# Optimization experiments

Measured on AMD Instinct MI355X. Metric: run time of the kernel, lower is better.

## Reference

```python
import jax, jax.numpy as jnp
import numpy as np

N, FIN, FOUT, H = 6144, 128, 64, 2
ALPHA = 0.2      # leaky relu slope
EPS = 1e-5       # layernorm eps
NEG = -9e15      # mask value from original code


def setup_inputs() -> dict:
    key = jax.random.key(0)
    k1, k2, k3, k4 = jax.random.split(key, 4)
    h = jax.random.normal(k1, (N, FIN), dtype=jnp.float32)
    adj = jax.random.randint(k2, (N, N), 0, 2, dtype=jnp.int32)
    # xavier_uniform over (fan_in, fan_out) of last two dims
    limW = float(np.sqrt(6.0 / (FIN + FOUT)))
    W = jax.random.uniform(k3, (H, FIN, FOUT), jnp.float32, -limW, limW)
    lima = float(np.sqrt(6.0 / (2 * FOUT + 1)))
    a = jax.random.uniform(k4, (H, 2 * FOUT, 1), jnp.float32, -lima, lima)
    gamma = jnp.ones((H * FOUT,), jnp.float32)
    beta = jnp.zeros((H * FOUT,), jnp.float32)
    return {"h": h, "adj": adj, "W": W, "a": a, "gamma": gamma, "beta": beta}


def reference(h, adj, W, a, gamma, beta):
    # h: [N, Fin], adj: [N, N] int, W: [H, Fin, Fout], a: [H, 2*Fout, 1]
    ht = jnp.einsum('ni,hio->hno', h, W)          # [H, N, Fout]
    a1 = a[:, :FOUT, 0]                            # [H, Fout]
    a2 = a[:, FOUT:, 0]                            # [H, Fout]
    # concat score a^T [h_i || h_j] == s1_i + s2_j (identical math, no NxNx2F tensor)
    s1 = jnp.einsum('hno,ho->hn', ht, a1)          # [H, N]
    s2 = jnp.einsum('hno,ho->hn', ht, a2)          # [H, N]
    e = s1[:, :, None] + s2[:, None, :]            # [H, N, N]
    e = jnp.where(e > 0, e, ALPHA * e)             # LeakyReLU
    e = jnp.where((adj > 0)[None], e, NEG)         # adjacency mask
    att = jax.nn.softmax(e, axis=-1)               # softmax over neighbors (dim=1 of [N,N])
    # dropout is identity in eval mode
    hp = jnp.einsum('hnm,hmo->hno', att, ht)       # [H, N, Fout]
    out = jnp.transpose(hp, (1, 0, 2)).reshape(N, H * FOUT)  # concat heads
    # LayerNorm(H*Fout), elementwise affine
    mu = out.mean(-1, keepdims=True)
    var = ((out - mu) ** 2).mean(-1, keepdims=True)
    out = (out - mu) / jnp.sqrt(var + EPS) * gamma + beta
    return out, att
```

## Files before the change

kernel.cpp:

```cpp
#include <hip/hip_runtime.h>
#include <hip/hip_bf16.h>

#define NNODES 6144
#define FIN    128
#define FOUTC  64
#define NHEAD  2
#define ALPHA  0.2f
#define LN_EPS 1e-5f
#define MASKW  192
#define LOG2E  1.4426950408889634f
#define INVN   (1.0f / 6144.0f)

typedef __attribute__((ext_vector_type(4))) float f32x4;
typedef __attribute__((ext_vector_type(8))) short short8;
typedef __attribute__((ext_vector_type(4))) int   i32x4;

static __device__ __forceinline__ short f2bf(float x) {
    unsigned u = __float_as_uint(x);
    u = (u + 0x7fffu + ((u >> 16) & 1u)) >> 16;
    return (short)u;
}

static __device__ __forceinline__ short f2bf_hw(float x) {
    return (short)__bfloat16_as_ushort(__float2bfloat16(x));
}

static __device__ __forceinline__ float ecalc2(float e, unsigned bit) {
    float m = fmaxf(e, ALPHA * e);
    return bit ? __builtin_amdgcn_exp2f(m) : 0.0f;
}
static __device__ __forceinline__ float pcalc2(float e, float li, unsigned bit,
                                               bool uni) {
    float m = fmaxf(e, ALPHA * e) + li;
    float t = bit ? __builtin_amdgcn_exp2f(m) : 0.0f;
    return uni ? INVN : t;
}

__global__ __launch_bounds__(256) void gat_k1(const float* __restrict__ h,
        const float* __restrict__ W, const float* __restrict__ a,
        short* __restrict__ htbP, float* __restrict__ s1, float* __restrict__ s2) {
    __shared__ float hrow[4][FIN];
    const int wid = threadIdx.x >> 6, lane = threadIdx.x & 63;
    const int n = blockIdx.x * 4 + wid;
    hrow[wid][lane]      = h[(size_t)n * FIN + lane];
    hrow[wid][lane + 64] = h[(size_t)n * FIN + lane + 64];
    __syncthreads();
    float acc0 = 0.f, acc1 = 0.f;
    #pragma unroll 8
    for (int k = 0; k < FIN; ++k) {
        float hv = hrow[wid][k];
        acc0 = fmaf(hv, W[k * FOUTC + lane], acc0);
        acc1 = fmaf(hv, W[(FIN + k) * FOUTC + lane], acc1);
    }
    const int it_ = n >> 5, kk = n & 31;
    const int fl  = (lane & 15) + ((kk >> 3) << 4);
    const size_t pb = ((size_t)(it_ * 4 + (lane >> 4))) * 512 + fl * 8 + (kk & 7);
    htbP[pb]          = f2bf(acc0);
    htbP[393216 + pb] = f2bf(acc1);
    float r00 = acc0 * a[lane];
    float r01 = acc0 * a[FOUTC + lane];
    float r10 = acc1 * a[2 * FOUTC + lane];
    float r11 = acc1 * a[3 * FOUTC + lane];
    #pragma unroll
    for (int off = 32; off; off >>= 1) {
        r00 += __shfl_xor(r00, off);
        r01 += __shfl_xor(r01, off);
        r10 += __shfl_xor(r10, off);
        r11 += __shfl_xor(r11, off);
    }
    if (lane == 0) {
        s1[n] = r00 * LOG2E;          s2[n] = r01 * LOG2E;
        s1[NNODES + n] = r10 * LOG2E; s2[NNODES + n] = r11 * LOG2E;
    }
}

__global__ __launch_bounds__(256) void gat_k2a(const int* __restrict__ adj,
        const float* __restrict__ s1, const float* __restrict__ s2,
        float* __restrict__ psum, unsigned* __restrict__ mask32) {
    const int n = blockIdx.x;
    const int t = threadIdx.x;
    const int wid = t >> 6, lane = t & 63;
    const i32x4* arow = (const i32x4*)(adj + (size_t)n * NNODES);
    const float4* s2h0 = (const float4*)(s2);
    const float4* s2h1 = (const float4*)(s2 + NNODES);
    const float s10 = s1[n], s11 = s1[NNODES + n];
    float sum0 = 0.f, sum1 = 0.f;
    unsigned* mrow = mask32 + (size_t)n * MASKW;
    #pragma unroll
    for (int i = 0; i < 6; ++i) {
        int c4 = t + i * 256;
        i32x4 av = __builtin_nontemporal_load(arow + c4);
        float4 sa = s2h0[c4];
        float4 sb = s2h1[c4];
        unsigned nib = (unsigned)(av[0] > 0) | ((unsigned)(av[1] > 0) << 1)
                     | ((unsigned)(av[2] > 0) << 2) | ((unsigned)(av[3] > 0) << 3);
        sum0 += (ecalc2(s10 + sa.x, nib & 1u) + ecalc2(s10 + sa.y, nib & 2u))
              + (ecalc2(s10 + sa.z, nib & 4u) + ecalc2(s10 + sa.w, nib & 8u));
        sum1 += (ecalc2(s11 + sb.x, nib & 1u) + ecalc2(s11 + sb.y, nib & 2u))
              + (ecalc2(s11 + sb.z, nib & 4u) + ecalc2(s11 + sb.w, nib & 8u));
        unsigned v = nib << ((lane & 7) * 4);
        v |= (unsigned)__shfl_xor((int)v, 1);
        v |= (unsigned)__shfl_xor((int)v, 2);
        v |= (unsigned)__shfl_xor((int)v, 4);
        if ((lane & 7) == 0)
            mrow[i * 32 + wid * 8 + (lane >> 3)] = v;
    }
    #pragma unroll
    for (int off = 32; off; off >>= 1) {
        sum0 += __shfl_xor(sum0, off);
        sum1 += __shfl_xor(sum1, off);
    }
    __shared__ float red[2][4];
    if (lane == 0) { red[0][wid] = sum0; red[1][wid] = sum1; }
    __syncthreads();
    if (t == 0) {
        psum[n]          = (red[0][0] + red[0][1]) + (red[0][2] + red[0][3]);
        psum[NNODES + n] = (red[1][0] + red[1][1]) + (red[1][2] + red[1][3]);
    }
}

template <int ITERS, int RATIO>
__global__ __launch_bounds__(256) void gat_mixed(const unsigned* __restrict__ mask32,
        const short* __restrict__ htbP, const float* __restrict__ s1,
        const float* __restrict__ s2, const float* __restrict__ psum,
        float* __restrict__ att, float* __restrict__ hpp) {
    const int bid = blockIdx.x;
    const int mid = bid / RATIO, rem = bid % RATIO;

    if (rem == RATIO - 1) {
        const int bx = (6144 / ITERS / 32 == 4) ? (mid & 1) : 0;
        const int by = (6144 / ITERS / 32 == 4) ? (mid >> 1) : mid;
        const int w = threadIdx.x >> 6, lane = threadIdx.x & 63;
        const int hh = w & 1, cs = w >> 1;
        const int pc = bx * 2 + cs;
        const int n0 = by * 16;
        const int r = lane & 15, g = lane >> 4;
        const int node = n0 + r;
        const float s1v = s1[hh * NNODES + node];
        const float ps  = psum[hh * NNODES + node];
        const bool uni = !(ps > 0.f);
        const float li = uni ? 0.f : -__log2f(ps);
        const float* s2h = s2 + hh * NNODES;
        const unsigned* mrow = mask32 + (size_t)node * MASKW + pc * ITERS;
        const short* bb = htbP + (size_t)(hh * 192 + pc * ITERS) * 2048 + (size_t)lane * 8;
        const int cbase = pc * ITERS * 32;

        f32x4 acc0 = {0.f,0.f,0.f,0.f}, acc1 = {0.f,0.f,0.f,0.f};
        f32x4 acc2 = {0.f,0.f,0.f,0.f}, acc3 = {0.f,0.f,0.f,0.f};

        #pragma unroll 4
        for (int it = 0; it < ITERS; ++it) {
            const int kb = cbase + it * 32 + g * 8;
            const unsigned mb = (mrow[it] >> (g * 8)) & 0xffu;
            float4 sa = *(const float4*)(s2h + kb);
            float4 sb = *(const float4*)(s2h + kb + 4);
            float p0 = pcalc2(s1v + sa.x, li, mb & 1u,   uni);
            float p1 = pcalc2(s1v + sa.y, li, mb & 2u,   uni);
            float p2 = pcalc2(s1v + sa.z, li, mb & 4u,   uni);
            float p3 = pcalc2(s1v + sa.w, li, mb & 8u,   uni);
            float p4 = pcalc2(s1v + sb.x, li, mb & 16u,  uni);
            float p5 = pcalc2(s1v + sb.y, li, mb & 32u,  uni);
            float p6 = pcalc2(s1v + sb.z, li, mb & 64u,  uni);
            float p7 = pcalc2(s1v + sb.w, li, mb & 128u, uni);
            short8 af = { f2bf_hw(p0), f2bf_hw(p1), f2bf_hw(p2), f2bf_hw(p3),
                          f2bf_hw(p4), f2bf_hw(p5), f2bf_hw(p6), f2bf_hw(p7) };
            const short* bp = bb + (size_t)it * 2048;
            short8 b0 = *(const short8*)(bp);
            short8 b1 = *(const short8*)(bp + 512);
            short8 b2 = *(const short8*)(bp + 1024);
            short8 b3 = *(const short8*)(bp + 1536);
            acc0 = __builtin_amdgcn_mfma_f32_16x16x32_bf16(af, b0, acc0, 0, 0, 0);
            acc1 = __builtin_amdgcn_mfma_f32_16x16x32_bf16(af, b1, acc1, 0, 0, 0);
            acc2 = __builtin_amdgcn_mfma_f32_16x16x32_bf16(af, b2, acc2, 0, 0, 0);
            acc3 = __builtin_amdgcn_mfma_f32_16x16x32_bf16(af, b3, acc3, 0, 0, 0);
        }
        float* hb = hpp + ((size_t)(pc * NHEAD + hh) * NNODES + (n0 + g * 4)) * FOUTC + r;
        #pragma unroll
        for (int reg = 0; reg < 4; ++reg) {
            hb[(size_t)reg * FOUTC +  0] = acc0[reg];
            hb[(size_t)reg * FOUTC + 16] = acc1[reg];
            hb[(size_t)reg * FOUTC + 32] = acc2[reg];
            hb[(size_t)reg * FOUTC + 48] = acc3[reg];
        }
    } else {
        const int idx = mid * (RATIO - 1) + rem;
        const int hh  = idx / NNODES;
        const int row = idx - hh * NNODES;
        const int t = threadIdx.x;
        const float ps = psum[hh * NNODES + row];
        float* attrow = att + ((size_t)hh * NNODES + row) * NNODES;
        if (!(ps > 0.f)) {
            const f32x4 u = {INVN, INVN, INVN, INVN};
            #pragma unroll
            for (int i = 0; i < 6; ++i)
                __builtin_nontemporal_store(u, (f32x4*)(attrow + i * 1024 + t * 4));
            return;
        }
        const float li = -__log2f(ps);
        const float s1v = s1[hh * NNODES + row];
        const float* s2h = s2 + hh * NNODES;
        const unsigned* mrow = mask32 + (size_t)row * MASKW;
        const int sh = (t & 7) * 4;
        #pragma unroll
        for (int i = 0; i < 6; ++i) {
            const int c0 = i * 1024 + t * 4;
            const unsigned bits = (mrow[c0 >> 5] >> sh) & 0xfu;
            float4 sv = *(const float4*)(s2h + c0);
            f32x4 st = { pcalc2(s1v + sv.x, li, bits & 1u, false),
                         pcalc2(s1v + sv.y, li, bits & 2u, false),
                         pcalc2(s1v + sv.z, li, bits & 4u, false),
                         pcalc2(s1v + sv.w, li, bits & 8u, false) };
            __builtin_nontemporal_store(st, (f32x4*)(attrow + c0));
        }
    }
}

__global__ __launch_bounds__(256) void gat_k4(const float* __restrict__ hpp,
        const float* __restrict__ gamma, const float* __restrict__ beta,
        float* __restrict__ out, int nchunk) {
    const int wid = threadIdx.x >> 6, lane = threadIdx.x & 63;
    const int n = blockIdx.x * 4 + wid;
    float v0 = 0.f, v1 = 0.f;
    for (int p = 0; p < nchunk; ++p) {
        v0 += hpp[((size_t)(p * NHEAD + 0) * NNODES + n) * FOUTC + lane];
        v1 += hpp[((size_t)(p * NHEAD + 1) * NNODES + n) * FOUTC + lane];
    }
    float s = v0 + v1;
    #pragma unroll
    for (int off = 32; off; off >>= 1) s += __shfl_xor(s, off);
    const float mu = s * (1.0f / 128.0f);
    const float d0 = v0 - mu, d1 = v1 - mu;
    float q = d0 * d0 + d1 * d1;
    #pragma unroll
    for (int off = 32; off; off >>= 1) q += __shfl_xor(q, off);
    const float rstd = 1.0f / sqrtf(q * (1.0f / 128.0f) + LN_EPS);
    out[(size_t)n * 128 + lane]      = d0 * rstd * gamma[lane] + beta[lane];
    out[(size_t)n * 128 + 64 + lane] = d1 * rstd * gamma[64 + lane] + beta[64 + lane];
}

extern "C" void kernel_launch(void* const* d_in, const int* in_sizes, int n_in,
                              void* d_out, int out_size, void* d_ws, size_t ws_size,
                              hipStream_t stream) {
    const float* h     = (const float*)d_in[0];
    const int*   adj   = (const int*)d_in[1];
    const float* W     = (const float*)d_in[2];
    const float* a     = (const float*)d_in[3];
    const float* gamma = (const float*)d_in[4];
    const float* beta  = (const float*)d_in[5];
    float* out = (float*)d_out;
    float* att = out + (size_t)NNODES * (NHEAD * FOUTC);

    char* ws = (char*)d_ws;
    short* htbP = (short*)ws;
    float* s1   = (float*)(ws + 1572864);
    float* s2p  = (float*)(ws + 1572864 + 49152);
    float* psum = (float*)(ws + 1572864 + 2 * 49152);
    unsigned* mask32 = (unsigned*)(ws + 1572864 + 3 * 49152);
    char* hpp_base = ws + 1572864 + 3 * 49152 + 4718592;
    size_t avail = (ws_size > 6438912) ? ws_size - 6438912 : 0;
    const size_t per_chunk = (size_t)NHEAD * NNODES * FOUTC * 4;
    const int nchunk = (avail >= 4 * per_chunk) ? 4 : 2;
    float* hpp = (float*)hpp_base;

    gat_k1<<<NNODES / 4, 256, 0, stream>>>(h, W, a, htbP, s1, s2p);
    gat_k2a<<<NNODES, 256, 0, stream>>>(adj, s1, s2p, psum, mask32);
    if (nchunk == 4) {
        gat_mixed<48, 17><<<13056, 256, 0, stream>>>(mask32, htbP, s1, s2p, psum, att, hpp);
    } else {
        gat_mixed<96, 33><<<12672, 256, 0, stream>>>(mask32, htbP, s1, s2p, psum, att, hpp);
    }
    gat_k4<<<NNODES / 4, 256, 0, stream>>>(hpp, gamma, beta, out, nchunk);
}
```

Baseline: 140.0 us.

## Store adjacency mask per-thread and process four attention rows per block

```diff
diff --git a/kernel.cpp b/kernel.cpp
--- a/kernel.cpp
+++ b/kernel.cpp
@@ -7,7 +7,6 @@
 #define NHEAD  2
 #define ALPHA  0.2f
 #define LN_EPS 1e-5f
-#define MASKW  192
 #define LOG2E  1.4426950408889634f
 #define INVN   (1.0f / 6144.0f)
 
@@ -76,7 +75,7 @@
 
 __global__ __launch_bounds__(256) void gat_k2a(const int* __restrict__ adj,
         const float* __restrict__ s1, const float* __restrict__ s2,
-        float* __restrict__ psum, unsigned* __restrict__ mask32) {
+        float* __restrict__ psum, unsigned* __restrict__ maskW2) {
     const int n = blockIdx.x;
     const int t = threadIdx.x;
     const int wid = t >> 6, lane = t & 63;
@@ -85,7 +84,7 @@
     const float4* s2h1 = (const float4*)(s2 + NNODES);
     const float s10 = s1[n], s11 = s1[NNODES + n];
     float sum0 = 0.f, sum1 = 0.f;
-    unsigned* mrow = mask32 + (size_t)n * MASKW;
+    unsigned myword = 0;
     #pragma unroll
     for (int i = 0; i < 6; ++i) {
         int c4 = t + i * 256;
@@ -98,13 +97,9 @@
               + (ecalc2(s10 + sa.z, nib & 4u) + ecalc2(s10 + sa.w, nib & 8u));
         sum1 += (ecalc2(s11 + sb.x, nib & 1u) + ecalc2(s11 + sb.y, nib & 2u))
               + (ecalc2(s11 + sb.z, nib & 4u) + ecalc2(s11 + sb.w, nib & 8u));
-        unsigned v = nib << ((lane & 7) * 4);
-        v |= (unsigned)__shfl_xor((int)v, 1);
-        v |= (unsigned)__shfl_xor((int)v, 2);
-        v |= (unsigned)__shfl_xor((int)v, 4);
-        if ((lane & 7) == 0)
-            mrow[i * 32 + wid * 8 + (lane >> 3)] = v;
-    }
+        myword |= nib << (4 * i);
+    }
+    maskW2[(size_t)n * 256 + t] = myword;
     #pragma unroll
     for (int off = 32; off; off >>= 1) {
         sum0 += __shfl_xor(sum0, off);
@@ -120,7 +115,7 @@
 }
 
 template <int ITERS, int RATIO>
-__global__ __launch_bounds__(256) void gat_mixed(const unsigned* __restrict__ mask32,
+__global__ __launch_bounds__(256) void gat_mixed(const unsigned* __restrict__ maskW2,
         const short* __restrict__ htbP, const float* __restrict__ s1,
         const float* __restrict__ s2, const float* __restrict__ psum,
         float* __restrict__ att, float* __restrict__ hpp) {
@@ -141,7 +136,7 @@
         const bool uni = !(ps > 0.f);
         const float li = uni ? 0.f : -__log2f(ps);
         const float* s2h = s2 + hh * NNODES;
-        const unsigned* mrow = mask32 + (size_t)node * MASKW + pc * ITERS;
+        const unsigned* mrowW = maskW2 + (size_t)node * 256;
         const short* bb = htbP + (size_t)(hh * 192 + pc * ITERS) * 2048 + (size_t)lane * 8;
         const int cbase = pc * ITERS * 32;
 
@@ -151,7 +146,9 @@
         #pragma unroll 4
         for (int it = 0; it < ITERS; ++it) {
             const int kb = cbase + it * 32 + g * 8;
-            const unsigned mb = (mrow[it] >> (g * 8)) & 0xffu;
+            const int t0 = (kb & 1023) >> 2, inib = (kb >> 10) * 4;
+            const unsigned w0 = mrowW[t0], w1 = mrowW[t0 + 1];
+            const unsigned mb = ((w0 >> inib) & 0xfu) | (((w1 >> inib) & 0xfu) << 4);
             float4 sa = *(const float4*)(s2h + kb);
             float4 sb = *(const float4*)(s2h + kb + 4);
             float p0 = pcalc2(s1v + sa.x, li, mb & 1u,   uni);
@@ -184,33 +181,36 @@
         }
     } else {
         const int idx = mid * (RATIO - 1) + rem;
-        const int hh  = idx / NNODES;
-        const int row = idx - hh * NNODES;
+        const int hh  = idx / 1536;
+        const int row0 = (idx - hh * 1536) * 4;
         const int t = threadIdx.x;
-        const float ps = psum[hh * NNODES + row];
-        float* attrow = att + ((size_t)hh * NNODES + row) * NNODES;
-        if (!(ps > 0.f)) {
-            const f32x4 u = {INVN, INVN, INVN, INVN};
-            #pragma unroll
-            for (int i = 0; i < 6; ++i)
-                __builtin_nontemporal_store(u, (f32x4*)(attrow + i * 1024 + t * 4));
-            return;
-        }
-        const float li = -__log2f(ps);
-        const float s1v = s1[hh * NNODES + row];
         const float* s2h = s2 + hh * NNODES;
-        const unsigned* mrow = mask32 + (size_t)row * MASKW;
-        const int sh = (t & 7) * 4;
+        float s1v[4], li[4];
+        bool uni[4];
+        unsigned mw[4];
+        #pragma unroll
+        for (int r = 0; r < 4; ++r) {
+            const float ps = psum[hh * NNODES + row0 + r];
+            uni[r] = !(ps > 0.f);
+            li[r]  = uni[r] ? 0.f : -__log2f(ps);
+            s1v[r] = s1[hh * NNODES + row0 + r];
+            mw[r]  = maskW2[(size_t)(row0 + r) * 256 + t];
+        }
+        float* attr = att + ((size_t)hh * NNODES + row0) * NNODES;
         #pragma unroll
         for (int i = 0; i < 6; ++i) {
             const int c0 = i * 1024 + t * 4;
-            const unsigned bits = (mrow[c0 >> 5] >> sh) & 0xfu;
             float4 sv = *(const float4*)(s2h + c0);
-            f32x4 st = { pcalc2(s1v + sv.x, li, bits & 1u, false),
-                         pcalc2(s1v + sv.y, li, bits & 2u, false),
-                         pcalc2(s1v + sv.z, li, bits & 4u, false),
-                         pcalc2(s1v + sv.w, li, bits & 8u, false) };
-            __builtin_nontemporal_store(st, (f32x4*)(attrow + c0));
+            #pragma unroll
+            for (int r = 0; r < 4; ++r) {
+                const unsigned bits = (mw[r] >> (4 * i)) & 0xfu;
+                f32x4 st = { pcalc2(s1v[r] + sv.x, li[r], bits & 1u, uni[r]),
+                             pcalc2(s1v[r] + sv.y, li[r], bits & 2u, uni[r]),
+                             pcalc2(s1v[r] + sv.z, li[r], bits & 4u, uni[r]),
+                             pcalc2(s1v[r] + sv.w, li[r], bits & 8u, uni[r]) };
+                __builtin_nontemporal_store(st,
+                    (f32x4*)(attr + (size_t)r * NNODES + c0));
+            }
         }
     }
 }
@@ -255,19 +255,19 @@
     float* s1   = (float*)(ws + 1572864);
     float* s2p  = (float*)(ws + 1572864 + 49152);
     float* psum = (float*)(ws + 1572864 + 2 * 49152);
-    unsigned* mask32 = (unsigned*)(ws + 1572864 + 3 * 49152);
-    char* hpp_base = ws + 1572864 + 3 * 49152 + 4718592;
-    size_t avail = (ws_size > 6438912) ? ws_size - 6438912 : 0;
+    unsigned* maskW2 = (unsigned*)(ws + 1572864 + 3 * 49152);
+    char* hpp_base = ws + 1572864 + 3 * 49152 + 6291456;
+    size_t avail = (ws_size > 8011776) ? ws_size - 8011776 : 0;
     const size_t per_chunk = (size_t)NHEAD * NNODES * FOUTC * 4;
     const int nchunk = (avail >= 4 * per_chunk) ? 4 : 2;
     float* hpp = (float*)hpp_base;
 
     gat_k1<<<NNODES / 4, 256, 0, stream>>>(h, W, a, htbP, s1, s2p);
-    gat_k2a<<<NNODES, 256, 0, stream>>>(adj, s1, s2p, psum, mask32);
+    gat_k2a<<<NNODES, 256, 0, stream>>>(adj, s1, s2p, psum, maskW2);
     if (nchunk == 4) {
-        gat_mixed<48, 17><<<13056, 256, 0, stream>>>(mask32, htbP, s1, s2p, psum, att, hpp);
+        gat_mixed<48, 5><<<3840, 256, 0, stream>>>(maskW2, htbP, s1, s2p, psum, att, hpp);
     } else {
-        gat_mixed<96, 33><<<12672, 256, 0, stream>>>(mask32, htbP, s1, s2p, psum, att, hpp);
+        gat_mixed<96, 9><<<3456, 256, 0, stream>>>(maskW2, htbP, s1, s2p, psum, att, hpp);
     }
     gat_k4<<<NNODES / 4, 256, 0, stream>>>(hpp, gamma, beta, out, nchunk);
 }
```

Result: slower. 156.7 us (+11.9%).
